# Performance work log

Measured on AMD Instinct MI355X. Metric: run time of the kernel, lower is better.

The kernel has to match this reference:

```python
import jax, jax.numpy as jnp
import numpy as np

B, S = 4096, 4096
NS, FDIM = 16, 64


def _ln(x, g, b):
    mu = jnp.mean(x, axis=-1, keepdims=True)
    v = jnp.mean((x - mu) ** 2, axis=-1, keepdims=True)
    return (x - mu) / jnp.sqrt(v + 1e-5) * g + b


def _rolling_vol_mean(returns, w):
    # mean over all length-w windows of unbiased std (matches per-window torch.std loop)
    Bn, L = returns.shape
    z = jnp.zeros((Bn, 1), returns.dtype)
    c1 = jnp.concatenate([z, jnp.cumsum(returns, axis=1)], axis=1)
    c2 = jnp.concatenate([z, jnp.cumsum(returns * returns, axis=1)], axis=1)
    s = c1[:, w:] - c1[:, :-w]    # [B, L-w+1] window sums
    s2 = c2[:, w:] - c2[:, :-w]
    var = (s2 - s * s / w) / (w - 1)
    return jnp.mean(jnp.sqrt(jnp.maximum(var, 0.0)), axis=1, keepdims=True)


def setup_inputs() -> dict:
    key = jax.random.key(0)
    ks = jax.random.split(key, 24)
    r = lambda i, shp: jax.random.normal(ks[i], shp, jnp.float32) * 0.05
    return {
        'price_series': jax.random.uniform(ks[0], (B, S, 1), jnp.float32) * 10.0 + 1.0,
        're_W': r(1, (4, 4, 64)), 're_b': r(2, (4, 64)),
        're_g': jnp.ones((4, 64), jnp.float32), 're_beta': jnp.zeros((4, 64), jnp.float32),
        'rh_W1': r(3, (256, 64)), 'rh_b1': r(4, (64,)), 'rh_W2': r(5, (64, 4)), 'rh_b2': r(6, (4,)),
        'rv_W': r(7, (3, 128)), 'rv_b': r(8, (128,)),
        'rv_g': jnp.ones((128,), jnp.float32), 'rv_beta': jnp.zeros((128,), jnp.float32),
        'vs_W': r(9, (128, 128)), 'vs_b': r(10, (128,)),
        'vs_g': jnp.ones((128,), jnp.float32), 'vs_beta': jnp.zeros((128,), jnp.float32),
        'vc_W1': r(11, (256, 64)), 'vc_b1': r(12, (64,)), 'vc_W2': r(13, (64, 4)), 'vc_b2': r(14, (4,)),
        'emb': r(15, (NS, FDIM)),
        'cn_W1': r(16, (576, 128)), 'cn_b1': r(17, (128,)),
        'cn_W2': r(18, (128, 64)), 'cn_b2': r(19, (64,)),
        'cn_W3': r(20, (64, 1)), 'cn_b3': r(21, (1,)),
    }


def reference(price_series, re_W, re_b, re_g, re_beta, rh_W1, rh_b1, rh_W2, rh_b2,
              rv_W, rv_b, rv_g, rv_beta, vs_W, vs_b, vs_g, vs_beta,
              vc_W1, vc_b1, vc_W2, vc_b2, emb, cn_W1, cn_b1, cn_W2, cn_b2, cn_W3, cn_b3):
    prices = price_series[:, :, 0]            # [B,S]
    Bn, Sn = prices.shape
    # --- MarketRegimeEncoder: SMA-20 via prefix sums (the per-step torch loop) ---
    cs = jnp.cumsum(prices, axis=1)
    shifted = jnp.concatenate([jnp.zeros((Bn, 20), prices.dtype), cs[:, :-20]], axis=1)
    counts = jnp.minimum(jnp.arange(Sn) + 1, 20).astype(prices.dtype)
    sma20 = (cs - shifted) / counts           # (sma_5 is computed but unused in original)
    trend = jnp.mean((prices - sma20) / (sma20 + 1e-8), axis=1, keepdims=True)
    p10 = prices[:, Sn - 10:Sn - 9]
    momentum = (prices[:, -1:] - p10) / (p10 + 1e-8)
    pmean = jnp.mean(prices, axis=1, keepdims=True)
    mean_rev = (prices[:, -1:] - pmean) / (pmean + 1e-8)
    pstd = jnp.std(prices, axis=1, keepdims=True, ddof=1)
    cycle = pstd / (pmean + 1e-8)
    combined = jnp.concatenate([trend, momentum, mean_rev, cycle], axis=1)  # [B,4]
    h = jax.nn.relu(jnp.einsum('bi,kio->bko', combined, re_W) + re_b[None])  # [B,4,64]
    h = _ln(h, re_g[None], re_beta[None])
    regime_features = h.reshape(Bn, -1)        # [B,256] (trend|momentum|mean_rev|cycle)
    logits = jax.nn.relu(regime_features @ rh_W1 + rh_b1) @ rh_W2 + rh_b2
    regime_probs = jax.nn.softmax(logits, axis=1)
    # --- VolatilityEncodingModule ---
    logp = jnp.log(jnp.maximum(price_series, 1e-8))
    returns = jnp.diff(logp, axis=1)[:, :, 0]  # [B,S-1]
    vol_in = jnp.concatenate([_rolling_vol_mean(returns, w) for w in (5, 10, 20)], axis=1)  # [B,3]
    rv = _ln(jax.nn.relu(vol_in @ rv_W + rv_b), rv_g, rv_beta)
    vs = _ln(jax.nn.relu(rv @ vs_W + vs_b), vs_g, vs_beta)
    vol_features = jnp.concatenate([rv, vs], axis=1)  # [B,256]
    vlogits = jax.nn.relu(vol_features @ vc_W1 + vc_b1) @ vc_W2 + vc_b2
    vol_regime = jax.nn.softmax(vlogits, axis=1)
    # --- OptionsStrategyEncoder: vectorized over strategies ---
    mv = jnp.concatenate([regime_features, vol_features], axis=1)  # [B,512]
    mvp = mv @ cn_W1[:512]                    # [B,128]
    ep = emb @ cn_W1[512:]                    # [NS,128]
    h1 = jax.nn.relu(mvp[:, None, :] + ep[None, :, :] + cn_b1)  # [B,NS,128]
    h2 = jax.nn.relu(h1 @ cn_W2 + cn_b2)      # [B,NS,64]
    scores = (h2 @ cn_W3 + cn_b3)[:, :, 0]    # [B,NS]
    return regime_features, regime_probs, vol_features, vol_regime, scores
```

## Files before the change

### kernel.cpp

```cpp
#include <hip/hip_runtime.h>
#include <math.h>

#define NROWS 4096
#define SLEN  4096
#define RETN  4095
#define STRD  274

__global__ __launch_bounds__(256) void k_ep(const float* __restrict__ emb,
                                            const float* __restrict__ cn_W1,
                                            const float* __restrict__ cn_b1,
                                            float* __restrict__ ep) {
    int idx = blockIdx.x * 256 + threadIdx.x;
    if (idx >= 16 * 128) return;
    int n = idx >> 7, o = idx & 127;
    float acc = cn_b1[o];
    const float* w = cn_W1 + 512 * 128;
    for (int i = 0; i < 64; ++i) acc = fmaf(emb[n * 64 + i], w[i * 128 + o], acc);
    ep[idx] = acc;
}

__global__ __launch_bounds__(256, 4) void k_stats(const float* __restrict__ price,
                                                  float* __restrict__ combined,
                                                  float* __restrict__ volin) {
    __shared__ float scm[16 * STRD];
    __shared__ float red[6][4];

    const int tid = threadIdx.x;
    const int row = blockIdx.x;
    const float* pr = price + (size_t)row * SLEN;

    float pA = 0.f, pB = 0.f;
    if (tid == 0) { pA = pr[SLEN - 10]; pB = pr[SLEN - 1]; }

    if (tid < 32) scm[(tid & 15) * STRD + (tid >> 4)] = 0.f;
    scm[(tid & 15) * STRD + 258 + (tid >> 4)] = 0.f;

    #pragma unroll
    for (int it = 0; it < 4; ++it) {
        const int i = it * 256 + tid;
        const float4 v = ((const float4*)pr)[i];
        const int base = (4 * (i & 3)) * STRD + (i >> 2) + 2;
        scm[base]            = v.x;
        scm[base + STRD]     = v.y;
        scm[base + 2 * STRD] = v.z;
        scm[base + 3 * STRD] = v.w;
    }
    __syncthreads();

    const int s0 = tid * 16;

    float hb[20];
    #pragma unroll
    for (int k = 0; k < 20; ++k)
        hb[k] = (k < 4) ? scm[(12 + k) * STRD + tid]
                        : scm[(k - 4) * STRD + (tid + 1)];
    float x_[16];
    #pragma unroll
    for (int d = 0; d < 16; ++d) x_[d] = scm[d * STRD + (tid + 2)];

    float W = 0.f;
    #pragma unroll
    for (int k = 0; k < 20; ++k) W += hb[k];
    float st = 0.f, s1p = 0.f, s2p = 0.f;
    #pragma unroll
    for (int d = 0; d < 16; ++d) {
        const float x = x_[d];
        W += x - hb[d];
        float inv_cnt = 0.05f;
        if (s0 == 0)                 inv_cnt = 1.0f / (float)(d + 1);
        else if (s0 == 16 && d < 3)  inv_cnt = 1.0f / (float)(17 + d);
        const float sma = W * inv_cnt;
        st  = fmaf(x - sma, __builtin_amdgcn_rcpf(sma + 1e-8f), st);
        s1p += x;
        s2p = fmaf(x, x, s2p);
    }

    float lg[17];
    #pragma unroll
    for (int d = 0; d < 16; ++d) lg[d] = __builtin_amdgcn_logf(fmaxf(x_[d], 1e-8f));
    lg[16] = __builtin_amdgcn_logf(fmaxf(scm[0 * STRD + (tid + 3)], 1e-8f));
    float rs[20];
    #pragma unroll
    for (int d = 0; d < 16; ++d) rs[d] = lg[d + 1] - lg[d];

    __syncthreads();

    #pragma unroll
    for (int d = 0; d < 16; ++d)
        if (s0 + d < RETN) scm[d * STRD + (tid + 2)] = rs[d];
    __syncthreads();

    #pragma unroll
    for (int j = 0; j < 4; ++j) rs[16 + j] = scm[j * STRD + (tid + 3)];

    float S5 = 0.f, Q5 = 0.f, S10 = 0.f, Q10 = 0.f, S20 = 0.f, Q20 = 0.f;
    #pragma unroll
    for (int j = 0; j < 20; ++j) {
        const float x = rs[j];
        S20 += x; Q20 = fmaf(x, x, Q20);
        if (j < 10) { S10 += x; Q10 = fmaf(x, x, Q10); }
        if (j < 5)  { S5  += x; Q5  = fmaf(x, x, Q5); }
    }

    #define SQT(S, Q, invw, invw1) \
        __builtin_amdgcn_sqrtf(fmaxf(fmaf(-(S) * (invw), (S), (Q)) * (invw1), 0.f))
    #define X5(d)  ((d) < 15 ? rs[(d) + 5]  : scm[4 * STRD + (tid + 3)])
    #define X10(d) ((d) < 10 ? rs[(d) + 10] : scm[((d) - 6) * STRD + (tid + 3)])
    #define X20(d) ((d) < 12 ? scm[((d) + 4) * STRD + (tid + 3)] \
                             : scm[((d) - 12) * STRD + (tid + 4)])

    float v5 = 0.f, v10 = 0.f, v20 = 0.f;
    if (tid < 254) {
        #pragma unroll
        for (int d = 0; d < 16; ++d) {
            v5  += SQT(S5,  Q5,  0.2f,  0.25f);
            v10 += SQT(S10, Q10, 0.1f,  1.f / 9.f);
            v20 += SQT(S20, Q20, 0.05f, 1.f / 19.f);
            const float xo = rs[d], qo = xo * xo;
            const float a5 = X5(d), a10 = X10(d), a20 = X20(d);
            S5  += a5  - xo;  Q5  = fmaf(a5,  a5,  Q5)  - qo;
            S10 += a10 - xo;  Q10 = fmaf(a10, a10, Q10) - qo;
            S20 += a20 - xo;  Q20 = fmaf(a20, a20, Q20) - qo;
        }
    } else {
        #pragma unroll
        for (int d = 0; d < 16; ++d) {
            const int i = s0 + d;
            if (i < 4091) v5  += SQT(S5,  Q5,  0.2f,  0.25f);
            if (i < 4086) v10 += SQT(S10, Q10, 0.1f,  1.f / 9.f);
            if (i < 4076) v20 += SQT(S20, Q20, 0.05f, 1.f / 19.f);
            const float xo = rs[d], qo = xo * xo;
            const float a5 = X5(d), a10 = X10(d), a20 = X20(d);
            S5  += a5  - xo;  Q5  = fmaf(a5,  a5,  Q5)  - qo;
            S10 += a10 - xo;  Q10 = fmaf(a10, a10, Q10) - qo;
            S20 += a20 - xo;  Q20 = fmaf(a20, a20, Q20) - qo;
        }
    }
    #undef SQT
    #undef X5
    #undef X10
    #undef X20

    {
        float vals[6] = {s1p, s2p, st, v5, v10, v20};
        const int lane = tid & 63, wid = tid >> 6;
        #pragma unroll
        for (int v = 0; v < 6; ++v) {
            float x = vals[v];
            for (int o = 32; o > 0; o >>= 1) x += __shfl_xor(x, o, 64);
            if (lane == 0) red[v][wid] = x;
        }
    }
    __syncthreads();
    if (tid == 0) {
        const float sum_p  = red[0][0] + red[0][1] + red[0][2] + red[0][3];
        const float sum_p2 = red[1][0] + red[1][1] + red[1][2] + red[1][3];
        const float sum_t  = red[2][0] + red[2][1] + red[2][2] + red[2][3];
        const float sv5    = red[3][0] + red[3][1] + red[3][2] + red[3][3];
        const float sv10   = red[4][0] + red[4][1] + red[4][2] + red[4][3];
        const float sv20   = red[5][0] + red[5][1] + red[5][2] + red[5][3];
        const float pmean = sum_p * (1.f / 4096.f);
        const float varp  = fmaf(-sum_p * (1.f / 4096.f), sum_p, sum_p2) * (1.f / 4095.f);
        const float pstd  = __builtin_amdgcn_sqrtf(fmaxf(varp, 0.f));
        const float ipm   = __builtin_amdgcn_rcpf(pmean + 1e-8f);
        combined[row * 4 + 0] = sum_t * (1.f / 4096.f);
        combined[row * 4 + 1] = (pB - pA) * __builtin_amdgcn_rcpf(pA + 1e-8f);
        combined[row * 4 + 2] = (pB - pmean) * ipm;
        combined[row * 4 + 3] = pstd * ipm;
        const float LN2 = 0.6931471805599453f;
        volin[row * 3 + 0] = sv5  * (LN2 / 4091.f);
        volin[row * 3 + 1] = sv10 * (LN2 / 4086.f);
        volin[row * 3 + 2] = sv20 * (LN2 / 4076.f);
    }
}

__global__ __launch_bounds__(256) void k_mlp(const float* __restrict__ combined,
                                             const float* __restrict__ volin,
                                             const float* __restrict__ re_W,  const float* __restrict__ re_b,
                                             const float* __restrict__ re_g,  const float* __restrict__ re_be,
                                             const float* __restrict__ rh_W1, const float* __restrict__ rh_b1,
                                             const float* __restrict__ rh_W2, const float* __restrict__ rh_b2,
                                             const float* __restrict__ rv_W,  const float* __restrict__ rv_b,
                                             const float* __restrict__ rv_g,  const float* __restrict__ rv_be,
                                             const float* __restrict__ vs_W,  const float* __restrict__ vs_b,
                                             const float* __restrict__ vs_g,  const float* __restrict__ vs_be,
                                             const float* __restrict__ vc_W1, const float* __restrict__ vc_b1,
                                             const float* __restrict__ vc_W2, const float* __restrict__ vc_b2,
                                             float* __restrict__ out_rf, float* __restrict__ out_rp,
                                             float* __restrict__ out_vf, float* __restrict__ out_vr) {
    __shared__ float rf_lds[8][256];
    __shared__ float vf_lds[8][256];
    __shared__ float ps[4][8][64];
    __shared__ float hid_s[8][64];
    __shared__ float prt[4][8];
    __shared__ float cmb_s[8][4];
    __shared__ float vol_s[8][3];

    const int tid  = threadIdx.x;
    const int lane = tid & 63;
    const int wid  = tid >> 6;
    const int row0 = blockIdx.x * 8;

    if (tid < 32) cmb_s[tid >> 2][tid & 3] = combined[(size_t)(row0 + (tid >> 2)) * 4 + (tid & 3)];
    else if (tid < 56) { int t = tid - 32; vol_s[t / 3][t % 3] = volin[(size_t)(row0 + t / 3) * 3 + t % 3]; }
    __syncthreads();

    {
        const float* w = re_W + wid * 256;
        const float w0 = w[lane], w1 = w[64 + lane], w2 = w[128 + lane], w3 = w[192 + lane];
        const float b  = re_b[wid * 64 + lane];
        const float gg = re_g[wid * 64 + lane], bb = re_be[wid * 64 + lane];
        float h[8], sm[8], sq[8];
        #pragma unroll
        for (int r = 0; r < 8; ++r) {
            float v = fmaf(cmb_s[r][0], w0, fmaf(cmb_s[r][1], w1,
                      fmaf(cmb_s[r][2], w2, fmaf(cmb_s[r][3], w3, b))));
            h[r] = fmaxf(v, 0.f);
            sm[r] = h[r]; sq[r] = h[r] * h[r];
        }
        #pragma unroll
        for (int off = 32; off > 0; off >>= 1) {
            #pragma unroll
            for (int r = 0; r < 8; ++r) {
                sm[r] += __shfl_xor(sm[r], off, 64);
                sq[r] += __shfl_xor(sq[r], off, 64);
            }
        }
        #pragma unroll
        for (int r = 0; r < 8; ++r) {
            const float mu  = sm[r] * (1.f / 64.f);
            const float var = fmaxf(sq[r] * (1.f / 64.f) - mu * mu, 0.f);
            const float y = (h[r] - mu) * rsqrtf(var + 1e-5f) * gg + bb;
            rf_lds[r][wid * 64 + lane] = y;
            out_rf[(size_t)(row0 + r) * 256 + wid * 64 + lane] = y;
        }
    }
    __syncthreads();

    {
        const int i0 = wid * 64;
        float acc[8] = {0.f, 0.f, 0.f, 0.f, 0.f, 0.f, 0.f, 0.f};
        for (int i = 0; i < 64; ++i) {
            const float wv = rh_W1[(size_t)(i0 + i) * 64 + lane];
            #pragma unroll
            for (int r = 0; r < 8; ++r) acc[r] = fmaf(rf_lds[r][i0 + i], wv, acc[r]);
        }
        #pragma unroll
        for (int r = 0; r < 8; ++r) ps[wid][r][lane] = acc[r];
    }
    __syncthreads();

    for (int it = tid; it < 512; it += 256) {
        const int r = it >> 6, o = it & 63;
        const float v = ps[0][r][o] + ps[1][r][o] + ps[2][r][o] + ps[3][r][o] + rh_b1[o];
        hid_s[r][o] = fmaxf(v, 0.f);
    }
    __syncthreads();

    if (tid < 32) {
        const int r = tid >> 2, j = tid & 3;
        float acc = rh_b2[j];
        for (int i = 0; i < 64; ++i) acc = fmaf(hid_s[r][i], rh_W2[i * 4 + j], acc);
        float m = acc;
        m = fmaxf(m, __shfl_xor(m, 1, 64));
        m = fmaxf(m, __shfl_xor(m, 2, 64));
        const float e = expf(acc - m);
        float s = e;
        s += __shfl_xor(s, 1, 64);
        s += __shfl_xor(s, 2, 64);
        out_rp[(size_t)(row0 + r) * 4 + j] = e / s;
    }

    {
        const int o = tid & 127, g = tid >> 7, wv_ = tid >> 6;
        const float w0 = rv_W[o], w1 = rv_W[128 + o], w2 = rv_W[256 + o];
        const float b = rv_b[o], gg = rv_g[o], bb = rv_be[o];
        float h[4], sm[4], sq[4];
        #pragma unroll
        for (int r4 = 0; r4 < 4; ++r4) {
            const int r = g * 4 + r4;
            float v = fmaf(vol_s[r][0], w0, fmaf(vol_s[r][1], w1, fmaf(vol_s[r][2], w2, b)));
            h[r4] = fmaxf(v, 0.f);
            sm[r4] = h[r4]; sq[r4] = h[r4] * h[r4];
        }
        #pragma unroll
        for (int off = 32; off > 0; off >>= 1) {
            #pragma unroll
            for (int r4 = 0; r4 < 4; ++r4) {
                sm[r4] += __shfl_xor(sm[r4], off, 64);
                sq[r4] += __shfl_xor(sq[r4], off, 64);
            }
        }
        if (lane == 0) {
            #pragma unroll
            for (int r4 = 0; r4 < 4; ++r4) { prt[wv_][r4 * 2] = sm[r4]; prt[wv_][r4 * 2 + 1] = sq[r4]; }
        }
        __syncthreads();
        #pragma unroll
        for (int r4 = 0; r4 < 4; ++r4) {
            const float S = prt[2 * g][2 * r4]     + prt[2 * g + 1][2 * r4];
            const float Q = prt[2 * g][2 * r4 + 1] + prt[2 * g + 1][2 * r4 + 1];
            const float mu  = S * (1.f / 128.f);
            const float var = fmaxf(Q * (1.f / 128.f) - mu * mu, 0.f);
            const float y = (h[r4] - mu) * rsqrtf(var + 1e-5f) * gg + bb;
            vf_lds[g * 4 + r4][o] = y;
            out_vf[(size_t)(row0 + g * 4 + r4) * 256 + o] = y;
        }
    }
    __syncthreads();

    {
        const int o = tid & 127, g = tid >> 7, wv_ = tid >> 6;
        float acc[4];
        const float b = vs_b[o];
        #pragma unroll
        for (int r4 = 0; r4 < 4; ++r4) acc[r4] = b;
        for (int i = 0; i < 128; ++i) {
            const float wv = vs_W[(size_t)i * 128 + o];
            #pragma unroll
            for (int r4 = 0; r4 < 4; ++r4) acc[r4] = fmaf(vf_lds[g * 4 + r4][i], wv, acc[r4]);
        }
        const float gg = vs_g[o], bb = vs_be[o];
        float h[4], sm[4], sq[4];
        #pragma unroll
        for (int r4 = 0; r4 < 4; ++r4) {
            h[r4] = fmaxf(acc[r4], 0.f);
            sm[r4] = h[r4]; sq[r4] = h[r4] * h[r4];
        }
        #pragma unroll
        for (int off = 32; off > 0; off >>= 1) {
            #pragma unroll
            for (int r4 = 0; r4 < 4; ++r4) {
                sm[r4] += __shfl_xor(sm[r4], off, 64);
                sq[r4] += __shfl_xor(sq[r4], off, 64);
            }
        }
        __syncthreads();
        if (lane == 0) {
            #pragma unroll
            for (int r4 = 0; r4 < 4; ++r4) { prt[wv_][r4 * 2] = sm[r4]; prt[wv_][r4 * 2 + 1] = sq[r4]; }
        }
        __syncthreads();
        #pragma unroll
        for (int r4 = 0; r4 < 4; ++r4) {
            const float S = prt[2 * g][2 * r4]     + prt[2 * g + 1][2 * r4];
            const float Q = prt[2 * g][2 * r4 + 1] + prt[2 * g + 1][2 * r4 + 1];
            const float mu  = S * (1.f / 128.f);
            const float var = fmaxf(Q * (1.f / 128.f) - mu * mu, 0.f);
            const float y = (h[r4] - mu) * rsqrtf(var + 1e-5f) * gg + bb;
            vf_lds[g * 4 + r4][128 + o] = y;
            out_vf[(size_t)(row0 + g * 4 + r4) * 256 + 128 + o] = y;
        }
    }
    __syncthreads();

    {
        const int i0 = wid * 64;
        float acc[8] = {0.f, 0.f, 0.f, 0.f, 0.f, 0.f, 0.f, 0.f};
        for (int i = 0; i < 64; ++i) {
            const float wv = vc_W1[(size_t)(i0 + i) * 64 + lane];
            #pragma unroll
            for (int r = 0; r < 8; ++r) acc[r] = fmaf(vf_lds[r][i0 + i], wv, acc[r]);
        }
        #pragma unroll
        for (int r = 0; r < 8; ++r) ps[wid][r][lane] = acc[r];
    }
    __syncthreads();

    for (int it = tid; it < 512; it += 256) {
        const int r = it >> 6, o = it & 63;
        const float v = ps[0][r][o] + ps[1][r][o] + ps[2][r][o] + ps[3][r][o] + vc_b1[o];
        hid_s[r][o] = fmaxf(v, 0.f);
    }
    __syncthreads();
    if (tid < 32) {
        const int r = tid >> 2, j = tid & 3;
        float acc = vc_b2[j];
        for (int i = 0; i < 64; ++i) acc = fmaf(hid_s[r][i], vc_W2[i * 4 + j], acc);
        float m = acc;
        m = fmaxf(m, __shfl_xor(m, 1, 64));
        m = fmaxf(m, __shfl_xor(m, 2, 64));
        const float e = expf(acc - m);
        float s = e;
        s += __shfl_xor(s, 1, 64);
        s += __shfl_xor(s, 2, 64);
        out_vr[(size_t)(row0 + r) * 4 + j] = e / s;
    }
}

__global__ __launch_bounds__(512, 6) void k_cross(const float* __restrict__ rfin,
                                                  const float* __restrict__ vfin,
                                                  const float* __restrict__ cn_W1,
                                                  const float* __restrict__ cn_W2,
                                                  const float* __restrict__ cn_b2,
                                                  const float* __restrict__ cn_W3,
                                                  const float* __restrict__ cn_b3,
                                                  const float* __restrict__ ep,
                                                  float* __restrict__ scores) {
    __shared__ __align__(16) float uni[4096];
    __shared__ __align__(16) float mvp_s[4][128];
    __shared__ __align__(16) float epb[16][132];

    const int tid  = threadIdx.x;
    const int lane = tid & 63;
    const int wv   = tid >> 6;
    const int row0 = blockIdx.x * 4;

    {
        const float* mvbase = (wv < 4)
            ? (rfin + (size_t)row0 * 256 + wv * 64)
            : (vfin + (size_t)row0 * 256 + (wv - 4) * 64);
        float acc0[4] = {0.f, 0.f, 0.f, 0.f};
        float acc1[4] = {0.f, 0.f, 0.f, 0.f};
        for (int ib = 0; ib < 64; ib += 4) {
            float4 m4[4];
            #pragma unroll
            for (int r = 0; r < 4; ++r) m4[r] = *(const float4*)(mvbase + r * 256 + ib);
            const float* w1p = cn_W1 + (size_t)(wv * 64 + ib) * 128 + lane;
            {   const float wa = w1p[0],   wb = w1p[64];
                #pragma unroll
                for (int r = 0; r < 4; ++r) { acc0[r] = fmaf(m4[r].x, wa, acc0[r]); acc1[r] = fmaf(m4[r].x, wb, acc1[r]); } }
            {   const float wa = w1p[128], wb = w1p[192];
                #pragma unroll
                for (int r = 0; r < 4; ++r) { acc0[r] = fmaf(m4[r].y, wa, acc0[r]); acc1[r] = fmaf(m4[r].y, wb, acc1[r]); } }
            {   const float wa = w1p[256], wb = w1p[320];
                #pragma unroll
                for (int r = 0; r < 4; ++r) { acc0[r] = fmaf(m4[r].z, wa, acc0[r]); acc1[r] = fmaf(m4[r].z, wb, acc1[r]); } }
            {   const float wa = w1p[384], wb = w1p[448];
                #pragma unroll
                for (int r = 0; r < 4; ++r) { acc0[r] = fmaf(m4[r].w, wa, acc0[r]); acc1[r] = fmaf(m4[r].w, wb, acc1[r]); } }
        }
        #pragma unroll
        for (int r = 0; r < 4; ++r) {
            uni[wv * 512 + r * 128 + lane]      = acc0[r];
            uni[wv * 512 + r * 128 + 64 + lane] = acc1[r];
        }
    }
    {
        const int ns = tid >> 5, c4 = (tid & 31) * 4;
        *(float4*)&epb[ns][c4] = *(const float4*)(ep + ns * 128 + c4);
    }
    __syncthreads();

    {
        const int r = tid >> 7, c = tid & 127;
        float s = 0.f;
        #pragma unroll
        for (int w = 0; w < 8; ++w) s += uni[w * 512 + r * 128 + c];
        mvp_s[r][c] = s;
    }
    __syncthreads();

    const int ch  = tid >> 8;
    const int nst = tid & 255;
    const int ns  = nst >> 4;
    const int t   = nst & 15;
    float acc[4][4];
    #pragma unroll
    for (int r = 0; r < 4; ++r)
        #pragma unroll
        for (int k = 0; k < 4; ++k) acc[r][k] = 0.f;
    {
        const int c0 = ch * 64;
        const float* W2c = cn_W2 + 4 * t;
        #pragma unroll 2
        for (int cb = 0; cb < 64; cb += 4) {
            const int c = c0 + cb;
            float4 m4[4];
            #pragma unroll
            for (int r = 0; r < 4; ++r) m4[r] = *(const float4*)&mvp_s[r][c];
            const float4 e4 = *(const float4*)&epb[ns][c];
            {   const float4 w2v = *(const float4*)(W2c + (size_t)(c + 0) * 64);
                #pragma unroll
                for (int r = 0; r < 4; ++r) {
                    const float h = fmaxf(m4[r].x + e4.x, 0.f);
                    acc[r][0] = fmaf(h, w2v.x, acc[r][0]); acc[r][1] = fmaf(h, w2v.y, acc[r][1]);
                    acc[r][2] = fmaf(h, w2v.z, acc[r][2]); acc[r][3] = fmaf(h, w2v.w, acc[r][3]); } }
            {   const float4 w2v = *(const float4*)(W2c + (size_t)(c + 1) * 64);
                #pragma unroll
                for (int r = 0; r < 4; ++r) {
                    const float h = fmaxf(m4[r].y + e4.y, 0.f);
                    acc[r][0] = fmaf(h, w2v.x, acc[r][0]); acc[r][1] = fmaf(h, w2v.y, acc[r][1]);
                    acc[r][2] = fmaf(h, w2v.z, acc[r][2]); acc[r][3] = fmaf(h, w2v.w, acc[r][3]); } }
            {   const float4 w2v = *(const float4*)(W2c + (size_t)(c + 2) * 64);
                #pragma unroll
                for (int r = 0; r < 4; ++r) {
                    const float h = fmaxf(m4[r].z + e4.z, 0.f);
                    acc[r][0] = fmaf(h, w2v.x, acc[r][0]); acc[r][1] = fmaf(h, w2v.y, acc[r][1]);
                    acc[r][2] = fmaf(h, w2v.z, acc[r][2]); acc[r][3] = fmaf(h, w2v.w, acc[r][3]); } }
            {   const float4 w2v = *(const float4*)(W2c + (size_t)(c + 3) * 64);
                #pragma unroll
                for (int r = 0; r < 4; ++r) {
                    const float h = fmaxf(m4[r].w + e4.w, 0.f);
                    acc[r][0] = fmaf(h, w2v.x, acc[r][0]); acc[r][1] = fmaf(h, w2v.y, acc[r][1]);
                    acc[r][2] = fmaf(h, w2v.z, acc[r][2]); acc[r][3] = fmaf(h, w2v.w, acc[r][3]); } }
        }
    }
    __syncthreads();
    if (ch == 1) {
        #pragma unroll
        for (int r = 0; r < 4; ++r)
            *(float4*)&uni[nst * 16 + r * 4] = make_float4(acc[r][0], acc[r][1], acc[r][2], acc[r][3]);
    }
    __syncthreads();
    if (ch == 0) {
        #pragma unroll
        for (int r = 0; r < 4; ++r) {
            const float4 o = *(const float4*)&uni[nst * 16 + r * 4];
            acc[r][0] += o.x; acc[r][1] += o.y; acc[r][2] += o.z; acc[r][3] += o.w;
        }
        const float4 b2v = *(const float4*)(cn_b2 + 4 * t);
        const float4 w3v = *(const float4*)(cn_W3 + 4 * t);
        const float  b3v = cn_b3[0];
        #pragma unroll
        for (int r = 0; r < 4; ++r) {
            float s =      fmaxf(acc[r][0] + b2v.x, 0.f) * w3v.x;
            s = fmaf(fmaxf(acc[r][1] + b2v.y, 0.f), w3v.y, s);
            s = fmaf(fmaxf(acc[r][2] + b2v.z, 0.f), w3v.z, s);
            s = fmaf(fmaxf(acc[r][3] + b2v.w, 0.f), w3v.w, s);
            s += __shfl_xor(s, 1, 64);
            s += __shfl_xor(s, 2, 64);
            s += __shfl_xor(s, 4, 64);
            s += __shfl_xor(s, 8, 64);
            if (t == 0) scores[(size_t)(row0 + r) * 16 + ns] = s + b3v;
        }
    }
}

extern "C" void kernel_launch(void* const* d_in, const int* in_sizes, int n_in,
                              void* d_out, int out_size, void* d_ws, size_t ws_size,
                              hipStream_t stream) {
    (void)in_sizes; (void)n_in; (void)out_size; (void)ws_size;

    const float* price = (const float*)d_in[0];
    const float* re_W  = (const float*)d_in[1];
    const float* re_b  = (const float*)d_in[2];
    const float* re_g  = (const float*)d_in[3];
    const float* re_be = (const float*)d_in[4];
    const float* rh_W1 = (const float*)d_in[5];
    const float* rh_b1 = (const float*)d_in[6];
    const float* rh_W2 = (const float*)d_in[7];
    const float* rh_b2 = (const float*)d_in[8];
    const float* rv_W  = (const float*)d_in[9];
    const float* rv_b  = (const float*)d_in[10];
    const float* rv_g  = (const float*)d_in[11];
    const float* rv_be = (const float*)d_in[12];
    const float* vs_W  = (const float*)d_in[13];
    const float* vs_b  = (const float*)d_in[14];
    const float* vs_g  = (const float*)d_in[15];
    const float* vs_be = (const float*)d_in[16];
    const float* vc_W1 = (const float*)d_in[17];
    const float* vc_b1 = (const float*)d_in[18];
    const float* vc_W2 = (const float*)d_in[19];
    const float* vc_b2 = (const float*)d_in[20];
    const float* emb   = (const float*)d_in[21];
    const float* cn_W1 = (const float*)d_in[22];
    const float* cn_b1 = (const float*)d_in[23];
    const float* cn_W2 = (const float*)d_in[24];
    const float* cn_b2 = (const float*)d_in[25];
    const float* cn_W3 = (const float*)d_in[26];
    const float* cn_b3 = (const float*)d_in[27];

    float* out    = (float*)d_out;
    float* out_rf = out;
    float* out_rp = out_rf + 4096 * 256;
    float* out_vf = out_rp + 4096 * 4;
    float* out_vr = out_vf + 4096 * 256;
    float* out_sc = out_vr + 4096 * 4;

    float* ws       = (float*)d_ws;
    float* combined = ws;
    float* volin    = combined + 4096 * 4;
    float* ep       = volin + 4096 * 3;

    hipLaunchKernelGGL(k_ep,    dim3(8),    dim3(256), 0, stream, emb, cn_W1, cn_b1, ep);
    hipLaunchKernelGGL(k_stats, dim3(4096), dim3(256), 0, stream, price, combined, volin);
    hipLaunchKernelGGL(k_mlp,   dim3(512),  dim3(256), 0, stream, combined, volin,
                       re_W, re_b, re_g, re_be, rh_W1, rh_b1, rh_W2, rh_b2,
                       rv_W, rv_b, rv_g, rv_be, vs_W, vs_b, vs_g, vs_be,
                       vc_W1, vc_b1, vc_W2, vc_b2,
                       out_rf, out_rp, out_vf, out_vr);
    hipLaunchKernelGGL(k_cross, dim3(1024), dim3(512), 0, stream, out_rf, out_vf,
                       cn_W1, cn_W2, cn_b2, cn_W3, cn_b3, ep, out_sc);
}
```

Measured before the change: 111.5 us.

## Stage W2 and mv rows in LDS, vectorize W1 loads in k_cross

```diff
diff --git a/kernel.cpp b/kernel.cpp
--- a/kernel.cpp
+++ b/kernel.cpp
@@ -388,7 +388,7 @@
     }
 }
 
-__global__ __launch_bounds__(512, 6) void k_cross(const float* __restrict__ rfin,
+__global__ __launch_bounds__(512, 4) void k_cross(const float* __restrict__ rfin,
                                                   const float* __restrict__ vfin,
                                                   const float* __restrict__ cn_W1,
                                                   const float* __restrict__ cn_W2,
@@ -397,7 +397,9 @@
                                                   const float* __restrict__ cn_b3,
                                                   const float* __restrict__ ep,
                                                   float* __restrict__ scores) {
+    __shared__ __align__(16) float w2s[128 * 64];
     __shared__ __align__(16) float uni[4096];
+    __shared__ __align__(16) float mvs[4][512];
     __shared__ __align__(16) float mvp_s[4][128];
     __shared__ __align__(16) float epb[16][132];
 
@@ -407,38 +409,53 @@
     const int row0 = blockIdx.x * 4;
 
     {
-        const float* mvbase = (wv < 4)
-            ? (rfin + (size_t)row0 * 256 + wv * 64)
-            : (vfin + (size_t)row0 * 256 + (wv - 4) * 64);
-        float acc0[4] = {0.f, 0.f, 0.f, 0.f};
-        float acc1[4] = {0.f, 0.f, 0.f, 0.f};
-        for (int ib = 0; ib < 64; ib += 4) {
-            float4 m4[4];
-            #pragma unroll
-            for (int r = 0; r < 4; ++r) m4[r] = *(const float4*)(mvbase + r * 256 + ib);
-            const float* w1p = cn_W1 + (size_t)(wv * 64 + ib) * 128 + lane;
-            {   const float wa = w1p[0],   wb = w1p[64];
-                #pragma unroll
-                for (int r = 0; r < 4; ++r) { acc0[r] = fmaf(m4[r].x, wa, acc0[r]); acc1[r] = fmaf(m4[r].x, wb, acc1[r]); } }
-            {   const float wa = w1p[128], wb = w1p[192];
-                #pragma unroll
-                for (int r = 0; r < 4; ++r) { acc0[r] = fmaf(m4[r].y, wa, acc0[r]); acc1[r] = fmaf(m4[r].y, wb, acc1[r]); } }
-            {   const float wa = w1p[256], wb = w1p[320];
-                #pragma unroll
-                for (int r = 0; r < 4; ++r) { acc0[r] = fmaf(m4[r].z, wa, acc0[r]); acc1[r] = fmaf(m4[r].z, wb, acc1[r]); } }
-            {   const float wa = w1p[384], wb = w1p[448];
-                #pragma unroll
-                for (int r = 0; r < 4; ++r) { acc0[r] = fmaf(m4[r].w, wa, acc0[r]); acc1[r] = fmaf(m4[r].w, wb, acc1[r]); } }
-        }
-        #pragma unroll
-        for (int r = 0; r < 4; ++r) {
-            uni[wv * 512 + r * 128 + lane]      = acc0[r];
-            uni[wv * 512 + r * 128 + 64 + lane] = acc1[r];
-        }
+        const int r = tid >> 7, cq = tid & 127;
+        const float* src = (cq < 64)
+            ? (rfin + (size_t)(row0 + r) * 256 + 4 * cq)
+            : (vfin + (size_t)(row0 + r) * 256 + 4 * (cq - 64));
+        *(float4*)&mvs[r][4 * cq] = *(const float4*)src;
+    }
+    #pragma unroll
+    for (int k = 0; k < 4; ++k) {
+        const int idx = k * 512 + tid;
+        *(float4*)&w2s[4 * idx] = *(const float4*)(cn_W2 + 4 * idx);
     }
     {
         const int ns = tid >> 5, c4 = (tid & 31) * 4;
         *(float4*)&epb[ns][c4] = *(const float4*)(ep + ns * 128 + c4);
+    }
+    __syncthreads();
+
+    {
+        const int p = lane >> 5;
+        const int q = lane & 31;
+        float acc[4][4] = {{0.f}};
+        const int ibase = wv * 64 + p;
+        #pragma unroll 8
+        for (int s = 0; s < 32; ++s) {
+            const int i = ibase + 2 * s;
+            const float4 w1v = *(const float4*)(cn_W1 + (size_t)i * 128 + 4 * q);
+            const float m0 = mvs[0][i], m1 = mvs[1][i], m2 = mvs[2][i], m3 = mvs[3][i];
+            acc[0][0] = fmaf(m0, w1v.x, acc[0][0]); acc[0][1] = fmaf(m0, w1v.y, acc[0][1]);
+            acc[0][2] = fmaf(m0, w1v.z, acc[0][2]); acc[0][3] = fmaf(m0, w1v.w, acc[0][3]);
+            acc[1][0] = fmaf(m1, w1v.x, acc[1][0]); acc[1][1] = fmaf(m1, w1v.y, acc[1][1]);
+            acc[1][2] = fmaf(m1, w1v.z, acc[1][2]); acc[1][3] = fmaf(m1, w1v.w, acc[1][3]);
+            acc[2][0] = fmaf(m2, w1v.x, acc[2][0]); acc[2][1] = fmaf(m2, w1v.y, acc[2][1]);
+            acc[2][2] = fmaf(m2, w1v.z, acc[2][2]); acc[2][3] = fmaf(m2, w1v.w, acc[2][3]);
+            acc[3][0] = fmaf(m3, w1v.x, acc[3][0]); acc[3][1] = fmaf(m3, w1v.y, acc[3][1]);
+            acc[3][2] = fmaf(m3, w1v.z, acc[3][2]); acc[3][3] = fmaf(m3, w1v.w, acc[3][3]);
+        }
+        #pragma unroll
+        for (int r = 0; r < 4; ++r) {
+            #pragma unroll
+            for (int k = 0; k < 4; ++k) acc[r][k] += __shfl_xor(acc[r][k], 32, 64);
+        }
+        if (p == 0) {
+            #pragma unroll
+            for (int r = 0; r < 4; ++r)
+                *(float4*)&uni[wv * 512 + r * 128 + 4 * q] =
+                    make_float4(acc[r][0], acc[r][1], acc[r][2], acc[r][3]);
+        }
     }
     __syncthreads();
 
@@ -462,7 +479,6 @@
         for (int k = 0; k < 4; ++k) acc[r][k] = 0.f;
     {
         const int c0 = ch * 64;
-        const float* W2c = cn_W2 + 4 * t;
         #pragma unroll 2
         for (int cb = 0; cb < 64; cb += 4) {
             const int c = c0 + cb;
@@ -470,25 +486,25 @@
             #pragma unroll
             for (int r = 0; r < 4; ++r) m4[r] = *(const float4*)&mvp_s[r][c];
             const float4 e4 = *(const float4*)&epb[ns][c];
-            {   const float4 w2v = *(const float4*)(W2c + (size_t)(c + 0) * 64);
+            {   const float4 w2v = *(const float4*)&w2s[(c + 0) * 64 + 4 * t];
                 #pragma unroll
                 for (int r = 0; r < 4; ++r) {
                     const float h = fmaxf(m4[r].x + e4.x, 0.f);
                     acc[r][0] = fmaf(h, w2v.x, acc[r][0]); acc[r][1] = fmaf(h, w2v.y, acc[r][1]);
                     acc[r][2] = fmaf(h, w2v.z, acc[r][2]); acc[r][3] = fmaf(h, w2v.w, acc[r][3]); } }
-            {   const float4 w2v = *(const float4*)(W2c + (size_t)(c + 1) * 64);
+            {   const float4 w2v = *(const float4*)&w2s[(c + 1) * 64 + 4 * t];
                 #pragma unroll
                 for (int r = 0; r < 4; ++r) {
                     const float h = fmaxf(m4[r].y + e4.y, 0.f);
                     acc[r][0] = fmaf(h, w2v.x, acc[r][0]); acc[r][1] = fmaf(h, w2v.y, acc[r][1]);
                     acc[r][2] = fmaf(h, w2v.z, acc[r][2]); acc[r][3] = fmaf(h, w2v.w, acc[r][3]); } }
-            {   const float4 w2v = *(const float4*)(W2c + (size_t)(c + 2) * 64);
+            {   const float4 w2v = *(const float4*)&w2s[(c + 2) * 64 + 4 * t];
                 #pragma unroll
                 for (int r = 0; r < 4; ++r) {
                     const float h = fmaxf(m4[r].z + e4.z, 0.f);
                     acc[r][0] = fmaf(h, w2v.x, acc[r][0]); acc[r][1] = fmaf(h, w2v.y, acc[r][1]);
                     acc[r][2] = fmaf(h, w2v.z, acc[r][2]); acc[r][3] = fmaf(h, w2v.w, acc[r][3]); } }
-            {   const float4 w2v = *(const float4*)(W2c + (size_t)(c + 3) * 64);
+            {   const float4 w2v = *(const float4*)&w2s[(c + 3) * 64 + 4 * t];
                 #pragma unroll
                 for (int r = 0; r < 4; ++r) {
                     const float h = fmaxf(m4[r].w + e4.w, 0.f);
```

New measurement: 100.6 us. 1.11x faster.
